# Optimization experiments

Measured on AMD Instinct MI355X. Metric: run time of the kernel, lower is better.

## Reference

```python
import jax, jax.numpy as jnp
import numpy as np

M, N, K, GROUP, BITS = 8192, 4096, 4096, 128, 4
NGROUPS = K // GROUP  # 32


def setup_inputs() -> dict:
    key = jax.random.key(0)
    k1, k2, k3, k4 = jax.random.split(key, 4)
    A = jax.random.normal(k1, (M, K), dtype=jnp.float32)
    # packed int4: each int32 entry holds one storage byte (two 4-bit nibbles), values 0..255
    qweight = jax.random.randint(k2, (N, K // 2), 0, 256, dtype=jnp.int32)
    scales = jax.random.uniform(k3, (N, NGROUPS), dtype=jnp.float32) * 0.02 + 0.001
    zeros = jax.random.randint(k4, (N, NGROUPS), 0, 16).astype(jnp.float32)
    return {"A": A, "qweight": qweight, "scales": scales, "zeros": zeros}


def dequantize(qweight, scales, zeros):
    # unpack two 4-bit nibbles per storage byte: col i of unpacked = (byte >> 4*(i%2)) & 0xF
    low = jnp.bitwise_and(qweight, 0xF)                      # [N, K//2]
    high = jnp.bitwise_and(qweight >> BITS, 0xF)             # [N, K//2]
    w = jnp.stack([low, high], axis=-1).reshape(N, K).astype(scales.dtype)  # interleaved, [N, K]
    # per-group dequant: (w - zero) * scale, group along K
    wg = w.reshape(N, NGROUPS, GROUP)
    wdq = (wg - zeros[:, :, None]) * scales[:, :, None]
    return wdq.reshape(N, K)


def reference(A, qweight, scales, zeros):
    W = dequantize(qweight, scales, zeros)  # [N, K]
    return jnp.einsum("mk,nk->mn", A, W)    # [M, N]
```

## Files before the change

### kernel.cpp

```cpp
#include <hip/hip_runtime.h>
#include <hip/hip_bf16.h>

typedef __bf16 bf16x8 __attribute__((ext_vector_type(8)));
typedef float  f32x4  __attribute__((ext_vector_type(4)));
typedef __attribute__((address_space(3))) char* lds3_t;

#define M_DIM 8192
#define N_DIM 4096
#define K_DIM 4096
#define NG    32
#define KHALF (K_DIM / 2)

__global__ __launch_bounds__(256) void cvtA_kernel(const float* __restrict__ A,
                                                   __bf16* __restrict__ Ab,
                                                   long n8) {
    long i = (long)blockIdx.x * blockDim.x + threadIdx.x;
    long stride = (long)gridDim.x * blockDim.x;
    const float4* A4 = (const float4*)A;
    for (long p = i; p < n8; p += stride) {
        float4 v0 = A4[2 * p];
        float4 v1 = A4[2 * p + 1];
        bf16x8 o;
        o[0] = (__bf16)v0.x; o[1] = (__bf16)v0.y;
        o[2] = (__bf16)v0.z; o[3] = (__bf16)v0.w;
        o[4] = (__bf16)v1.x; o[5] = (__bf16)v1.y;
        o[6] = (__bf16)v1.z; o[7] = (__bf16)v1.w;
        *(bf16x8*)(Ab + p * 8) = o;
    }
}

__global__ __launch_bounds__(256) void deqW_kernel(const int* __restrict__ qw,
                                                   const float* __restrict__ sc,
                                                   const float* __restrict__ zr,
                                                   __bf16* __restrict__ Wb) {
    long i = (long)blockIdx.x * blockDim.x + threadIdx.x;
    long stride = (long)gridDim.x * blockDim.x;
    const long nch = (long)N_DIM * (KHALF / 4);
    const int4* q4 = (const int4*)qw;
    for (long p = i; p < nch; p += stride) {
        int n  = (int)(p >> 9);
        int cj = (int)(p & 511);
        int i0 = cj * 4;
        int g  = i0 >> 6;
        float s = sc[n * NG + g];
        float z = zr[n * NG + g];
        int4 qv = q4[p];
        bf16x8 o;
        int b;
        b = qv.x; o[0] = (__bf16)(((float)(b & 0xF) - z) * s);
                  o[1] = (__bf16)(((float)((b >> 4) & 0xF) - z) * s);
        b = qv.y; o[2] = (__bf16)(((float)(b & 0xF) - z) * s);
                  o[3] = (__bf16)(((float)((b >> 4) & 0xF) - z) * s);
        b = qv.z; o[4] = (__bf16)(((float)(b & 0xF) - z) * s);
                  o[5] = (__bf16)(((float)((b >> 4) & 0xF) - z) * s);
        b = qv.w; o[6] = (__bf16)(((float)(b & 0xF) - z) * s);
                  o[7] = (__bf16)(((float)((b >> 4) & 0xF) - z) * s);
        *(bf16x8*)(Wb + (long)n * K_DIM + i0 * 2) = o;
    }
}

#define BM 256
#define BN 256
#define BK 64
#define NT (K_DIM / BK)

#define SB0 __builtin_amdgcn_sched_barrier(0)
#define BAR do { SB0; __builtin_amdgcn_s_barrier(); } while (0)
#define LGKM(N) do { asm volatile("s_waitcnt lgkmcnt(" #N ")" ::: "memory"); SB0; } while (0)
#define VMW(N)  do { asm volatile("s_waitcnt vmcnt(" #N ")"  ::: "memory"); SB0; } while (0)
#define PRIO1 __builtin_amdgcn_s_setprio(1)
#define PRIO0 __builtin_amdgcn_s_setprio(0)

#define DSR(dst, base, OFFS) \
    asm volatile("ds_read_b128 %0, %1 offset:" OFFS : "=v"(dst) : "v"(base))

#define RD_A(BASEV, Q, K, O0, O1, O2, O3)          \
  do {                                             \
    DSR(a##Q##k##K[0], BASEV, O0);                 \
    DSR(a##Q##k##K[1], BASEV, O1);                 \
    DSR(a##Q##k##K[2], BASEV, O2);                 \
    DSR(a##Q##k##K[3], BASEV, O3);                 \
  } while (0)

#define RD_B(BASEV, Q, K, O0, O1)                  \
  do {                                             \
    DSR(b##Q##k##K[0], BASEV, O0);                 \
    DSR(b##Q##k##K[1], BASEV, O1);                 \
  } while (0)

#define ACC1(QM, MM, QN, NN, KK)                                                 \
  acc[(QM) * 4 + (MM)][(QN) * 2 + (NN)] = __builtin_amdgcn_mfma_f32_16x16x32_bf16( \
      a##QM##k##KK[MM], b##QN##k##KK[NN], acc[(QM) * 4 + (MM)][(QN) * 2 + (NN)], 0, 0, 0)

#define MFMA8(QM, QN, KK)       \
  do {                          \
    PRIO1;                      \
    ACC1(QM, 0, QN, 0, KK);     \
    ACC1(QM, 0, QN, 1, KK);     \
    ACC1(QM, 1, QN, 0, KK);     \
    ACC1(QM, 1, QN, 1, KK);     \
    ACC1(QM, 2, QN, 0, KK);     \
    ACC1(QM, 2, QN, 1, KK);     \
    ACC1(QM, 3, QN, 0, KK);     \
    ACC1(QM, 3, QN, 1, KK);     \
    PRIO0;                      \
  } while (0)

#define STAGE(SRC, MATOFF, H, DB, KT)                                                              \
  do {                                                                                             \
    __builtin_amdgcn_global_load_lds(                                                              \
        (__attribute__((address_space(1))) void*)((SRC) + (long)((H) * 128) * (K_DIM * 2) +        \
                                                  (long)(KT) * (BK * 2)),                          \
        (__attribute__((address_space(3))) void*)(lds + (DB) + (MATOFF) + (H) * 16384 + ldst),     \
        16, 0, 0);                                                                                 \
    __builtin_amdgcn_global_load_lds(                                                              \
        (__attribute__((address_space(1))) void*)((SRC) + (long)((H) * 128 + 64) * (K_DIM * 2) +   \
                                                  (long)(KT) * (BK * 2)),                          \
        (__attribute__((address_space(3))) void*)(lds + (DB) + (MATOFF) + (H) * 16384 + 8192 +     \
                                                  ldst),                                           \
        16, 0, 0);                                                                                 \
  } while (0)

#define TILE(P, PN, JJ)                                                           \
  do {                                                                            \
    const int jp1 = (JJ) + 1, jp2 = (JJ) + 2;                                     \
                               \
    BAR;                                                                          \
    RD_A(aa##P##0, 1, 0, "8192", "10240", "12288", "14336");                      \
    if (jp1 < NT) STAGE(Bsrc, 32768, 0, (PN) * 65536, jp1);                       \
    LGKM(4);                                                                      \
    MFMA8(0, 0, 0);                                                               \
                               \
    BAR;                                                                          \
    RD_B(ba##P##0, 1, 0, "4096", "6144");                                         \
    if (jp1 < NT) STAGE(Bsrc, 32768, 1, (PN) * 65536, jp1);                       \
    LGKM(2);                                                                      \
    MFMA8(1, 0, 0);                                                               \
                                                           \
    BAR;                                                                          \
    LGKM(0);                                                                      \
    MFMA8(1, 1, 0);                                                               \
                                         \
    BAR;                                                                          \
    RD_A(aa##P##1, 0, 1, "0", "2048", "4096", "6144");                            \
    RD_B(ba##P##1, 1, 1, "4096", "6144");                                         \
    LGKM(6);                                                                      \
    MFMA8(0, 1, 0);                                                               \
                                                \
    BAR;                                                                          \
    RD_A(aa##P##1, 1, 1, "8192", "10240", "12288", "14336");                      \
    LGKM(4);                                                                      \
    MFMA8(0, 1, 1);                                                               \
                                                \
    BAR;                                                                          \
    RD_B(ba##P##1, 0, 1, "0", "2048");                                            \
    LGKM(2);                                                                      \
    MFMA8(1, 1, 1);                                                               \
                                   \
    BAR;                                                                          \
    LGKM(0);                                                                      \
    if (jp2 < NT) {                                                               \
      STAGE(Asrc, 0, 0, (P) * 65536, jp2);                                        \
      VMW(2);                                                                     \
    } else {                                                                      \
      VMW(0);                                                                     \
    }                                                                             \
    MFMA8(1, 0, 1);                                                               \
         \
    BAR;                                                                          \
    RD_A(aa##PN##0, 0, 0, "0", "2048", "4096", "6144");                           \
    RD_B(ba##PN##0, 0, 0, "0", "2048");                                           \
    if (jp2 < NT) STAGE(Asrc, 0, 1, (P) * 65536, jp2);                            \
    LGKM(6);                                                                      \
    MFMA8(0, 0, 1);                                                               \
  } while (0)

__global__ __launch_bounds__(512, 2) void gemm8p(const __bf16* __restrict__ A,
                                                 const __bf16* __restrict__ B,
                                                 float* __restrict__ C) {
    __shared__ __attribute__((aligned(128))) char lds[131072];

    const int nwg = (M_DIM / BM) * (N_DIM / BN);
    int bid = blockIdx.x;
    int sw  = (bid & 7) * (nwg >> 3) + (bid >> 3);
    int mt = sw >> 4, ntl = sw & 15;
    int bm0 = mt * BM, bn0 = ntl * BN;

    int tid  = threadIdx.x;
    int lane = tid & 63;
    int wid  = tid >> 6;
    int wr   = wid >> 2;
    int wc   = wid & 3;

    f32x4 acc[8][4];
    f32x4 vz = {0.f, 0.f, 0.f, 0.f};
#pragma unroll
    for (int m = 0; m < 8; ++m)
#pragma unroll
        for (int n = 0; n < 4; ++n) acc[m][n] = vz;

    bf16x8 a0k0[4], a1k0[4], a0k1[4], a1k1[4];
    bf16x8 b0k0[2], b1k0[2], b0k1[2], b1k1[2];

    int srow  = tid >> 3;
    int scolb = ((tid & 7) ^ (srow & 7)) * 16;
    const char* Asrc = (const char*)(A + (long)(bm0 + srow) * K_DIM) + scolb;
    const char* Bsrc = (const char*)(B + (long)(bn0 + srow) * K_DIM) + scolb;
    int ldst = tid * 16;

    int lrow = lane & 15;
    int rc0  = (((lane >> 4) ^ (lane & 7)) << 4);
    int rc1  = rc0 ^ 64;
    int aoff = wr * 16384 + lrow * 128;
    int boff = 32768 + (wc >> 1) * 16384 + ((wc & 1) * 64 + lrow) * 128;

    lds3_t aa00 = (lds3_t)(lds + aoff + rc0);
    lds3_t aa01 = (lds3_t)(lds + aoff + rc1);
    lds3_t aa10 = (lds3_t)(lds + 65536 + aoff + rc0);
    lds3_t aa11 = (lds3_t)(lds + 65536 + aoff + rc1);
    lds3_t ba00 = (lds3_t)(lds + boff + rc0);
    lds3_t ba01 = (lds3_t)(lds + boff + rc1);
    lds3_t ba10 = (lds3_t)(lds + 65536 + boff + rc0);
    lds3_t ba11 = (lds3_t)(lds + 65536 + boff + rc1);

    STAGE(Asrc, 0,     0, 0, 0);
    STAGE(Asrc, 0,     1, 0, 0);
    STAGE(Bsrc, 32768, 0, 0, 0);
    STAGE(Bsrc, 32768, 1, 0, 0);
    STAGE(Asrc, 0,     0, 65536, 1);
    STAGE(Asrc, 0,     1, 65536, 1);
    VMW(4);
    BAR;
    RD_A(aa00, 0, 0, "0", "2048", "4096", "6144");
    RD_B(ba00, 0, 0, "0", "2048");

    for (int j = 0; j < NT; j += 2) {
        TILE(0, 1, j);
        TILE(1, 0, j + 1);
    }

    int crow0 = bm0 + wr * 128 + (lane >> 4) * 4;
    int ccol0 = bn0 + wc * 64 + (lane & 15);
#pragma unroll
    for (int m = 0; m < 8; ++m)
#pragma unroll
        for (int n = 0; n < 4; ++n) {
            long base = (long)(crow0 + m * 16) * N_DIM + (ccol0 + n * 16);
#pragma unroll
            for (int jj = 0; jj < 4; ++jj)
                C[base + (long)jj * N_DIM] = acc[m][n][jj];
        }
}

__global__ __launch_bounds__(256) void gemm_fallback(const float* __restrict__ A,
                                                     const int* __restrict__ qw,
                                                     const float* __restrict__ sc,
                                                     const float* __restrict__ zr,
                                                     float* __restrict__ C) {
    __shared__ float Ash[16][17];
    __shared__ float Wsh[16][17];
    int tx = threadIdx.x & 15, ty = threadIdx.x >> 4;
    int m = blockIdx.y * 16 + ty;
    int n = blockIdx.x * 16 + tx;
    float s = 0.f;
    for (int k0 = 0; k0 < K_DIM; k0 += 16) {
        Ash[ty][tx] = A[(long)m * K_DIM + k0 + tx];
        {
            int nn = blockIdx.x * 16 + ty;
            int kk = k0 + tx;
            int q = qw[(long)nn * KHALF + (kk >> 1)];
            int nib = (kk & 1) ? ((q >> 4) & 0xF) : (q & 0xF);
            int g = kk >> 7;
            Wsh[ty][tx] = ((float)nib - zr[nn * NG + g]) * sc[nn * NG + g];
        }
        __syncthreads();
#pragma unroll
        for (int kk = 0; kk < 16; ++kk)
            s += Ash[ty][kk] * Wsh[tx][kk];
        __syncthreads();
    }
    C[(long)m * N_DIM + n] = s;
}

extern "C" void kernel_launch(void* const* d_in, const int* in_sizes, int n_in,
                              void* d_out, int out_size, void* d_ws, size_t ws_size,
                              hipStream_t stream) {
    const float* A  = (const float*)d_in[0];
    const int*   qw = (const int*)d_in[1];
    const float* sc = (const float*)d_in[2];
    const float* zr = (const float*)d_in[3];
    float* C = (float*)d_out;

    const size_t needA = (size_t)M_DIM * K_DIM * 2;
    const size_t needW = (size_t)N_DIM * K_DIM * 2;

    if (ws_size >= needA + needW) {
        __bf16* Ab = (__bf16*)d_ws;
        __bf16* Wb = (__bf16*)((char*)d_ws + needA);
        cvtA_kernel<<<2048, 256, 0, stream>>>(A, Ab, (long)M_DIM * K_DIM / 8);
        deqW_kernel<<<2048, 256, 0, stream>>>(qw, sc, zr, Wb);
        gemm8p<<<(M_DIM / BM) * (N_DIM / BN), 512, 0, stream>>>(Ab, Wb, C);
    } else {
        dim3 g(N_DIM / 16, M_DIM / 16);
        gemm_fallback<<<g, 256, 0, stream>>>(A, qw, sc, zr, C);
    }
}
```

Baseline: 277.2 us.

## Switch GEMM inner loop from 16x16x32 to 32x32x16 bf16 MFMA tiles

Replaces the 16x16x32 MFMA instructions with 32x32x16 MFMA, halving the number of matrix instructions per wave tile and changing the accumulator layout to 16-wide vectors. The LDS read addressing is reworked so each read computes its swizzled address with an inline v_xor, using a single base pointer per buffer instead of separate precomputed bases. The epilogue store mapping is rewritten for the 32x32 output layout. The aim is higher MFMA throughput and fewer operand reads per FLOP, at the cost of extra VALU xor instructions and possibly different LDS bank-conflict behaviour.

```diff
diff --git a/kernel.cpp b/kernel.cpp
--- a/kernel.cpp
+++ b/kernel.cpp
@@ -3,6 +3,7 @@
 
 typedef __bf16 bf16x8 __attribute__((ext_vector_type(8)));
 typedef float  f32x4  __attribute__((ext_vector_type(4)));
+typedef float  f32x16 __attribute__((ext_vector_type(16)));
 typedef __attribute__((address_space(3))) char* lds3_t;
 
 #define M_DIM 8192
@@ -71,39 +72,40 @@
 #define PRIO1 __builtin_amdgcn_s_setprio(1)
 #define PRIO0 __builtin_amdgcn_s_setprio(0)
 
-#define DSR(dst, base, OFFS) \
-    asm volatile("ds_read_b128 %0, %1 offset:" OFFS : "=v"(dst) : "v"(base))
-
-#define RD_A(BASEV, Q, K, O0, O1, O2, O3)          \
+#define DSRX(dst, base, XR, OFFS)                                        \
+  do {                                                                   \
+    unsigned _t_;                                                        \
+    asm volatile("v_xor_b32 %1, " XR ", %2\n\t"                          \
+                 "ds_read_b128 %0, %1 offset:" OFFS                      \
+                 : "=v"(dst), "=&v"(_t_) : "v"(base));                   \
+  } while (0)
+
+#define RD_A(BASE, Q, K, X0, X1, O0, O1)           \
   do {                                             \
-    DSR(a##Q##k##K[0], BASEV, O0);                 \
-    DSR(a##Q##k##K[1], BASEV, O1);                 \
-    DSR(a##Q##k##K[2], BASEV, O2);                 \
-    DSR(a##Q##k##K[3], BASEV, O3);                 \
-  } while (0)
-
-#define RD_B(BASEV, Q, K, O0, O1)                  \
+    DSRX(a##Q##k##K[0], BASE, X0, O0);             \
+    DSRX(a##Q##k##K[1], BASE, X1, O0);             \
+    DSRX(a##Q##k##K[2], BASE, X0, O1);             \
+    DSRX(a##Q##k##K[3], BASE, X1, O1);             \
+  } while (0)
+
+#define RD_B(BASE, Q, K, X0, X1, ON)               \
   do {                                             \
-    DSR(b##Q##k##K[0], BASEV, O0);                 \
-    DSR(b##Q##k##K[1], BASEV, O1);                 \
-  } while (0)
-
-#define ACC1(QM, MM, QN, NN, KK)                                                 \
-  acc[(QM) * 4 + (MM)][(QN) * 2 + (NN)] = __builtin_amdgcn_mfma_f32_16x16x32_bf16( \
-      a##QM##k##KK[MM], b##QN##k##KK[NN], acc[(QM) * 4 + (MM)][(QN) * 2 + (NN)], 0, 0, 0)
-
-#define MFMA8(QM, QN, KK)       \
-  do {                          \
-    PRIO1;                      \
-    ACC1(QM, 0, QN, 0, KK);     \
-    ACC1(QM, 0, QN, 1, KK);     \
-    ACC1(QM, 1, QN, 0, KK);     \
-    ACC1(QM, 1, QN, 1, KK);     \
-    ACC1(QM, 2, QN, 0, KK);     \
-    ACC1(QM, 2, QN, 1, KK);     \
-    ACC1(QM, 3, QN, 0, KK);     \
-    ACC1(QM, 3, QN, 1, KK);     \
-    PRIO0;                      \
+    DSRX(b##Q##k##K[0], BASE, X0, ON);             \
+    DSRX(b##Q##k##K[1], BASE, X1, ON);             \
+  } while (0)
+
+#define MFMA4(QM, QN, KK)                                                          \
+  do {                                                                             \
+    PRIO1;                                                                         \
+    acc[(QM) * 2 + 0][QN] = __builtin_amdgcn_mfma_f32_32x32x16_bf16(               \
+        a##QM##k##KK[0], b##QN##k##KK[0], acc[(QM) * 2 + 0][QN], 0, 0, 0);         \
+    acc[(QM) * 2 + 0][QN] = __builtin_amdgcn_mfma_f32_32x32x16_bf16(               \
+        a##QM##k##KK[1], b##QN##k##KK[1], acc[(QM) * 2 + 0][QN], 0, 0, 0);         \
+    acc[(QM) * 2 + 1][QN] = __builtin_amdgcn_mfma_f32_32x32x16_bf16(               \
+        a##QM##k##KK[2], b##QN##k##KK[0], acc[(QM) * 2 + 1][QN], 0, 0, 0);         \
+    acc[(QM) * 2 + 1][QN] = __builtin_amdgcn_mfma_f32_32x32x16_bf16(               \
+        a##QM##k##KK[3], b##QN##k##KK[1], acc[(QM) * 2 + 1][QN], 0, 0, 0);         \
+    PRIO0;                                                                         \
   } while (0)
 
 #define STAGE(SRC, MATOFF, H, DB, KT)                                                              \
@@ -126,36 +128,36 @@
     const int jp1 = (JJ) + 1, jp2 = (JJ) + 2;                                     \
                                \
     BAR;                                                                          \
-    RD_A(aa##P##0, 1, 0, "8192", "10240", "12288", "14336");                      \
+    RD_A(aa##P, 1, 0, "0", "32", "8192", "12288");                                \
     if (jp1 < NT) STAGE(Bsrc, 32768, 0, (PN) * 65536, jp1);                       \
     LGKM(4);                                                                      \
-    MFMA8(0, 0, 0);                                                               \
+    MFMA4(0, 0, 0);                                                               \
                                \
     BAR;                                                                          \
-    RD_B(ba##P##0, 1, 0, "4096", "6144");                                         \
+    RD_B(ba##P, 1, 0, "0", "32", "4096");                                         \
     if (jp1 < NT) STAGE(Bsrc, 32768, 1, (PN) * 65536, jp1);                       \
     LGKM(2);                                                                      \
-    MFMA8(1, 0, 0);                                                               \
+    MFMA4(1, 0, 0);                                                               \
                                                            \
     BAR;                                                                          \
     LGKM(0);                                                                      \
-    MFMA8(1, 1, 0);                                                               \
+    MFMA4(1, 1, 0);                                                               \
                                          \
     BAR;                                                                          \
-    RD_A(aa##P##1, 0, 1, "0", "2048", "4096", "6144");                            \
-    RD_B(ba##P##1, 1, 1, "4096", "6144");                                         \
+    RD_A(aa##P, 0, 1, "64", "96", "0", "4096");                                   \
+    RD_B(ba##P, 1, 1, "64", "96", "4096");                                        \
     LGKM(6);                                                                      \
-    MFMA8(0, 1, 0);                                                               \
+    MFMA4(0, 1, 0);                                                               \
                                                 \
     BAR;                                                                          \
-    RD_A(aa##P##1, 1, 1, "8192", "10240", "12288", "14336");                      \
+    RD_A(aa##P, 1, 1, "64", "96", "8192", "12288");                               \
     LGKM(4);                                                                      \
-    MFMA8(0, 1, 1);                                                               \
+    MFMA4(0, 1, 1);                                                               \
                                                 \
     BAR;                                                                          \
-    RD_B(ba##P##1, 0, 1, "0", "2048");                                            \
+    RD_B(ba##P, 0, 1, "64", "96", "0");                                           \
     LGKM(2);                                                                      \
-    MFMA8(1, 1, 1);                                                               \
+    MFMA4(1, 1, 1);                                                               \
                                    \
     BAR;                                                                          \
     LGKM(0);                                                                      \
@@ -165,14 +167,14 @@
     } else {                                                                      \
       VMW(0);                                                                     \
     }                                                                             \
-    MFMA8(1, 0, 1);                                                               \
+    MFMA4(1, 0, 1);                                                               \
          \
     BAR;                                                                          \
-    RD_A(aa##PN##0, 0, 0, "0", "2048", "4096", "6144");                           \
-    RD_B(ba##PN##0, 0, 0, "0", "2048");                                           \
+    RD_A(aa##PN, 0, 0, "0", "32", "0", "4096");                                   \
+    RD_B(ba##PN, 0, 0, "0", "32", "0");                                           \
     if (jp2 < NT) STAGE(Asrc, 0, 1, (P) * 65536, jp2);                            \
     LGKM(6);                                                                      \
-    MFMA8(0, 0, 1);                                                               \
+    MFMA4(0, 0, 1);                                                               \
   } while (0)
 
 __global__ __launch_bounds__(512, 2) void gemm8p(const __bf16* __restrict__ A,
@@ -192,12 +194,13 @@
     int wr   = wid >> 2;
     int wc   = wid & 3;
 
-    f32x4 acc[8][4];
-    f32x4 vz = {0.f, 0.f, 0.f, 0.f};
-#pragma unroll
-    for (int m = 0; m < 8; ++m)
-#pragma unroll
-        for (int n = 0; n < 4; ++n) acc[m][n] = vz;
+    f32x16 acc[4][2];
+#pragma unroll
+    for (int m = 0; m < 4; ++m)
+#pragma unroll
+        for (int n = 0; n < 2; ++n)
+#pragma unroll
+            for (int r = 0; r < 16; ++r) acc[m][n][r] = 0.f;
 
     bf16x8 a0k0[4], a1k0[4], a0k1[4], a1k1[4];
     bf16x8 b0k0[2], b1k0[2], b0k1[2], b1k1[2];
@@ -208,20 +211,12 @@
     const char* Bsrc = (const char*)(B + (long)(bn0 + srow) * K_DIM) + scolb;
     int ldst = tid * 16;
 
-    int lrow = lane & 15;
-    int rc0  = (((lane >> 4) ^ (lane & 7)) << 4);
-    int rc1  = rc0 ^ 64;
-    int aoff = wr * 16384 + lrow * 128;
-    int boff = 32768 + (wc >> 1) * 16384 + ((wc & 1) * 64 + lrow) * 128;
-
-    lds3_t aa00 = (lds3_t)(lds + aoff + rc0);
-    lds3_t aa01 = (lds3_t)(lds + aoff + rc1);
-    lds3_t aa10 = (lds3_t)(lds + 65536 + aoff + rc0);
-    lds3_t aa11 = (lds3_t)(lds + 65536 + aoff + rc1);
-    lds3_t ba00 = (lds3_t)(lds + boff + rc0);
-    lds3_t ba01 = (lds3_t)(lds + boff + rc1);
-    lds3_t ba10 = (lds3_t)(lds + 65536 + boff + rc0);
-    lds3_t ba11 = (lds3_t)(lds + 65536 + boff + rc1);
+    int cs0  = (((lane >> 5) ^ (lane & 7)) << 4);
+    int arow = (lane & 31) * 128;
+    lds3_t aa0 = (lds3_t)(lds + wr * 16384 + arow + cs0);
+    lds3_t aa1 = (lds3_t)(lds + 65536 + wr * 16384 + arow + cs0);
+    lds3_t ba0 = (lds3_t)(lds + 32768 + wc * 8192 + arow + cs0);
+    lds3_t ba1 = (lds3_t)(lds + 65536 + 32768 + wc * 8192 + arow + cs0);
 
     STAGE(Asrc, 0,     0, 0, 0);
     STAGE(Asrc, 0,     1, 0, 0);
@@ -231,25 +226,25 @@
     STAGE(Asrc, 0,     1, 65536, 1);
     VMW(4);
     BAR;
-    RD_A(aa00, 0, 0, "0", "2048", "4096", "6144");
-    RD_B(ba00, 0, 0, "0", "2048");
+    RD_A(aa0, 0, 0, "0", "32", "0", "4096");
+    RD_B(ba0, 0, 0, "0", "32", "0");
 
     for (int j = 0; j < NT; j += 2) {
         TILE(0, 1, j);
         TILE(1, 0, j + 1);
     }
 
-    int crow0 = bm0 + wr * 128 + (lane >> 4) * 4;
-    int ccol0 = bn0 + wc * 64 + (lane & 15);
-#pragma unroll
-    for (int m = 0; m < 8; ++m)
-#pragma unroll
-        for (int n = 0; n < 4; ++n) {
-            long base = (long)(crow0 + m * 16) * N_DIM + (ccol0 + n * 16);
-#pragma unroll
-            for (int jj = 0; jj < 4; ++jj)
-                C[base + (long)jj * N_DIM] = acc[m][n][jj];
-        }
+    int crow0 = bm0 + wr * 128 + ((lane >> 5) << 2);
+    int ccol0 = bn0 + wc * 64 + (lane & 31);
+#pragma unroll
+    for (int mb = 0; mb < 4; ++mb)
+#pragma unroll
+        for (int nb = 0; nb < 2; ++nb)
+#pragma unroll
+            for (int r = 0; r < 16; ++r) {
+                int row = mb * 32 + (r & 3) + ((r >> 2) << 3);
+                C[(long)(crow0 + row) * N_DIM + (ccol0 + nb * 32)] = acc[mb][nb][r];
+            }
 }
 
 __global__ __launch_bounds__(256) void gemm_fallback(const float* __restrict__ A,
```

After: 313.2 us. 13.0% more time.
